# Performance work log

Hardware: AMD Instinct MI355X
Metric: run time of the kernel (lower is better)

## Reference

```python
import jax, jax.numpy as jnp
import numpy as np

B, T, I, H, L = 8192, 256, 28, 10, 2


def setup_inputs() -> dict:
    key = jax.random.key(0)
    ks = jax.random.split(key, 10)
    s_ih0 = 1.0 / np.sqrt(H)
    return {
        "x": jax.random.normal(ks[0], (B, T, I), dtype=jnp.float32),
        "h0": jnp.zeros((L, B, H), dtype=jnp.float32),
        "W_ih_l0": jax.random.uniform(ks[1], (H, I), minval=-s_ih0, maxval=s_ih0),
        "W_hh_l0": jax.random.uniform(ks[2], (H, H), minval=-s_ih0, maxval=s_ih0),
        "b_ih_l0": jax.random.uniform(ks[3], (H,), minval=-s_ih0, maxval=s_ih0),
        "b_hh_l0": jax.random.uniform(ks[4], (H,), minval=-s_ih0, maxval=s_ih0),
        "W_ih_l1": jax.random.uniform(ks[5], (H, H), minval=-s_ih0, maxval=s_ih0),
        "W_hh_l1": jax.random.uniform(ks[6], (H, H), minval=-s_ih0, maxval=s_ih0),
        "b_ih_l1": jax.random.uniform(ks[7], (H,), minval=-s_ih0, maxval=s_ih0),
        "b_hh_l1": jax.random.uniform(ks[8], (H,), minval=-s_ih0, maxval=s_ih0),
    }


def reference(x, h0, W_ih_l0, W_hh_l0, b_ih_l0, b_hh_l0,
              W_ih_l1, W_hh_l1, b_ih_l1, b_hh_l1):
    # torch RNN (tanh): h_t = tanh(x_t @ W_ih^T + b_ih + h_{t-1} @ W_hh^T + b_hh)
    # Precompute layer-0 input projections for all timesteps (big GEMM up front).
    xw0 = jnp.einsum('bti,hi->tbh', x, W_ih_l0) + (b_ih_l0 + b_hh_l0)  # [T,B,H]
    b1 = b_ih_l1 + b_hh_l1

    def step(carry, xw0_t):
        h_0, h_1 = carry
        h_0 = jnp.tanh(xw0_t + h_0 @ W_hh_l0.T)
        h_1 = jnp.tanh(h_0 @ W_ih_l1.T + b1 + h_1 @ W_hh_l1.T)
        return (h_0, h_1), h_1

    (hT_0, hT_1), out_tbh = jax.lax.scan(step, (h0[0], h0[1]), xw0)
    output = jnp.transpose(out_tbh, (1, 0, 2))          # [B,T,H] (batch_first)
    h_final = jnp.stack([hT_0, hT_1], axis=0)           # [2,B,H]
    return output, h_final
```

## Files before the change

### kernel.cpp

```cpp
#include <hip/hip_runtime.h>

#define B_ 8192
#define T_ 256
#define I_ 28
#define H_ 10

#define OUT_MAIN (B_ * T_ * H_)
#define BH (B_ * H_)

typedef __bf16 bf16x8 __attribute__((ext_vector_type(8)));
typedef float f32x16 __attribute__((ext_vector_type(16)));
typedef float f32x4  __attribute__((ext_vector_type(4)));
union W4u { unsigned int w[4]; bf16x8 v; };

__device__ __forceinline__ float fast_tanh(float x) {
    float e = __builtin_amdgcn_exp2f(x * 2.885390081777927f);
    return __builtin_fmaf(-2.0f, __builtin_amdgcn_rcpf(e + 1.0f), 1.0f);
}

__device__ __forceinline__ unsigned short f2bf(float f) {
    unsigned u = __float_as_uint(f);
    unsigned r = ((u >> 16) & 1) + 0x7fff;
    return (unsigned short)((u + r) >> 16);
}

__device__ __forceinline__ void cvtpair(float f0, float f1, unsigned& dh, unsigned& dl) {
    asm("v_cvt_pk_bf16_f32 %0, %1, %2" : "=v"(dh) : "v"(f0), "v"(f1));
    float r0 = f0 - __uint_as_float(dh << 16);
    float r1 = f1 - __uint_as_float(dh & 0xffff0000u);
    asm("v_cvt_pk_bf16_f32 %0, %1, %2" : "=v"(dl) : "v"(r0), "v"(r1));
}

#define REBUILD(vv0,vv1,vv2,vv3,vv4,vv5, DST) { \
    unsigned t01, t23, t45, w3 = 0; \
    asm("v_cvt_pk_bf16_f32 %0, %1, %2" : "=v"(t01) : "v"(vv0), "v"(vv1)); \
    asm("v_cvt_pk_bf16_f32 %0, %1, %2" : "=v"(t23) : "v"(vv2), "v"(vv3)); \
    asm("v_cvt_pk_bf16_f32 %0, %1, %2" : "=v"(t45) : "v"(vv4), "v"(vv5)); \
    asm volatile("s_nop 1" : "+v"(t01), "+v"(t23), "+v"(t45)); \
    asm("v_permlane32_swap_b32 %0, %1" : "+v"(t01), "+v"(t45)); \
    asm("v_permlane32_swap_b32 %0, %1" : "+v"(t23), "+v"(w3)); \
    W4u nb_; nb_.w[0]=t01; nb_.w[1]=t23; nb_.w[2]=t45; nb_.w[3]=w3; \
    DST = nb_.v; }

#define GLD4o(dst, addr, OFF) \
    asm volatile("global_load_dwordx4 %0, %1, off offset:" #OFF : "=v"(dst) : "v"(addr));

#define LOADX(SA, SB, SC, SD, tt) { \
    const float* a0_ = xrow + (long)(tt) * I_ + 8 * h; \
    const float* a1_ = xrow + (long)(tt) * I_ + 20; \
    GLD4o(SA, a0_, 0) \
    GLD4o(SB, a0_, 16) \
    GLD4o(SC, a0_, 64) \
    GLD4o(SD, a1_, 0) }

#define WAITX(SA, SB, SC, SD, N) \
    asm volatile("s_waitcnt vmcnt(" #N ")" : "+v"(SA), "+v"(SB), "+v"(SC), "+v"(SD));

#define MAKEXC(SA, SB, SC, SD) { \
    W4u xhA, xlA, xhB, xlB; \
    cvtpair(SA[0], SA[1], xhA.w[0], xlA.w[0]); \
    cvtpair(SA[2], SA[3], xhA.w[1], xlA.w[1]); \
    cvtpair(SB[0], SB[1], xhA.w[2], xlA.w[2]); \
    cvtpair(SB[2], SB[3], xhA.w[3], xlA.w[3]); \
    cvtpair(SC[0], SC[1], xhB.w[0], xlB.w[0]); \
    cvtpair(SC[2], SC[3], xhB.w[1], xlB.w[1]); \
    cvtpair(SD[0], SD[1], xhB.w[2], xlB.w[2]); \
    cvtpair(SD[2], SD[3], xhB.w[3], xlB.w[3]); \
    f32x16 xcA = __builtin_amdgcn_mfma_f32_32x32x16_bf16(Axh0, xlA.v, C0SEED, 0,0,0); \
    f32x16 xcB = __builtin_amdgcn_mfma_f32_32x32x16_bf16(Axl0, xhA.v, ZERO16, 0,0,0); \
    f32x16 xcC = __builtin_amdgcn_mfma_f32_32x32x16_bf16(Axh0, xhA.v, ZERO16, 0,0,0); \
    xcA = __builtin_amdgcn_mfma_f32_32x32x16_bf16(Axh1, xlB.v, xcA, 0,0,0); \
    xcB = __builtin_amdgcn_mfma_f32_32x32x16_bf16(Axl1, xhB.v, xcB, 0,0,0); \
    xcC = __builtin_amdgcn_mfma_f32_32x32x16_bf16(Axh1, xhB.v, xcC, 0,0,0); \
    XC[0]=xcA[0]+xcB[0]+xcC[0]; XC[1]=xcA[1]+xcB[1]+xcC[1]; \
    XC[2]=xcA[2]+xcB[2]+xcC[2]; XC[3]=xcA[3]+xcB[3]+xcC[3]; \
    XC[4]=xcA[4]+xcB[4]+xcC[4]; XC[5]=xcA[5]+xcB[5]+xcC[5]; }

#define STEP(s8, PA,PB,PC,PD, NA,NB,NC,ND) { \
    int t = tb + (s8); \
    f32x16 c1a = __builtin_amdgcn_mfma_f32_32x32x16_bf16(Ahh1, Bh1, C1SEED, 0,0,0); \
    f32x16 c0  = __builtin_amdgcn_mfma_f32_32x32x16_bf16(Ahh0, Bh0, XC, 0,0,0); \
    WAITX(NA,NB,NC,ND, 8) \
    v0 = fast_tanh(c0[0]); v1 = fast_tanh(c0[1]); v2 = fast_tanh(c0[2]); \
    v3 = fast_tanh(c0[3]); v4 = fast_tanh(c0[4]); v5 = fast_tanh(c0[5]); \
    REBUILD(v0,v1,v2,v3,v4,v5, Bh0) \
    f32x16 c1 = __builtin_amdgcn_mfma_f32_32x32x16_bf16(Aih1, Bh0, c1a, 0,0,0); \
    MAKEXC(NA,NB,NC,ND) \
    g0 = fast_tanh(c1[0]); g1 = fast_tanh(c1[1]); g2 = fast_tanh(c1[2]); \
    g3 = fast_tanh(c1[3]); g4 = fast_tanh(c1[4]); g5 = fast_tanh(c1[5]); \
    float* op = orow + t * H_; \
    *(float4*)(op + xo) = make_float4(g0, g1, g2, g3); \
    if (!h) *(float2*)(op + 8) = make_float2(g4, g5); \
    REBUILD(g0,g1,g2,g3,g4,g5, Bh1) \
    int tl = (t + 4 < T_) ? (t + 4) : (T_ - 1); \
    LOADX(PA,PB,PC,PD, tl) }

__global__ __launch_bounds__(64)
__attribute__((amdgpu_waves_per_eu(1, 1)))
void rnn_fused(const float* __restrict__ x, const float* __restrict__ h0in,
               const float* __restrict__ Wih0, const float* __restrict__ Whh0,
               const float* __restrict__ bih0, const float* __restrict__ bhh0,
               const float* __restrict__ Wih1, const float* __restrict__ Whh1,
               const float* __restrict__ bih1, const float* __restrict__ bhh1,
               float* __restrict__ out, float* __restrict__ hfin) {
    const int l = threadIdx.x;
    const int n = l & 31, h = l >> 5;
    const int bb = blockIdx.x * 32;
    const int am = n;

    W4u a0u, aiu, ahu;
#pragma unroll
    for (int jj = 0; jj < 4; jj++) {
        int k0 = 8*h + 2*jj, k1 = k0 + 1;
        bool r0 = (am < H_) && (k0 < H_), r1 = (am < H_) && (k1 < H_);
        unsigned lo, hi;
        lo = r0 ? f2bf(Whh0[am*H_+k0]) : 0u; hi = r1 ? f2bf(Whh0[am*H_+k1]) : 0u;
        a0u.w[jj] = lo | (hi<<16);
        lo = r0 ? f2bf(Wih1[am*H_+k0]) : 0u; hi = r1 ? f2bf(Wih1[am*H_+k1]) : 0u;
        aiu.w[jj] = lo | (hi<<16);
        lo = r0 ? f2bf(Whh1[am*H_+k0]) : 0u; hi = r1 ? f2bf(Whh1[am*H_+k1]) : 0u;
        ahu.w[jj] = lo | (hi<<16);
    }
    bf16x8 Ahh0 = a0u.v, Aih1 = aiu.v, Ahh1 = ahu.v;
    asm volatile("" : "+v"(Ahh0), "+v"(Aih1), "+v"(Ahh1));

    W4u xh0u, xh1u, xl0u, xl1u;
#pragma unroll
    for (int s = 0; s < 2; s++) {
#pragma unroll
        for (int jj = 0; jj < 4; jj++) {
            int k0 = 16*s + 8*h + 2*jj, k1 = k0 + 1;
            unsigned short h0b=0, h1b=0, l0b=0, l1b=0;
            if (am < H_ && k0 < I_) {
                float f = Wih0[am*I_+k0];
                h0b = f2bf(f);
                l0b = f2bf(f - __uint_as_float(((unsigned)h0b)<<16));
            }
            if (am < H_ && k1 < I_) {
                float f = Wih0[am*I_+k1];
                h1b = f2bf(f);
                l1b = f2bf(f - __uint_as_float(((unsigned)h1b)<<16));
            }
            unsigned wh = (unsigned)h0b | ((unsigned)h1b<<16);
            unsigned wl = (unsigned)l0b | ((unsigned)l1b<<16);
            if (s==0) { xh0u.w[jj]=wh; xl0u.w[jj]=wl; }
            else      { xh1u.w[jj]=wh; xl1u.w[jj]=wl; }
        }
    }
    bf16x8 Axh0 = xh0u.v, Axh1 = xh1u.v, Axl0 = xl0u.v, Axl1 = xl1u.v;
    asm volatile("" : "+v"(Axh0), "+v"(Axh1), "+v"(Axl0), "+v"(Axl1));

    f32x16 C0SEED, C1SEED, ZERO16;
#pragma unroll
    for (int r = 0; r < 16; r++) { C0SEED[r] = 0.f; C1SEED[r] = 0.f; ZERO16[r] = 0.f; }
#pragma unroll
    for (int r = 0; r < 6; r++) {
        int mm = (r & 3) + 8 * (r >> 2) + 4 * h;
        if (mm < H_) {
            C0SEED[r] = bih0[mm] + bhh0[mm];
            C1SEED[r] = bih1[mm] + bhh1[mm];
        }
    }
    asm volatile("" : "+v"(C0SEED), "+v"(C1SEED), "+v"(ZERO16));

    W4u b0u, b1u;
#pragma unroll
    for (int jj = 0; jj < 4; jj++) {
        int k0 = 8*h + 2*jj, k1 = k0 + 1;
        float f0 = (k0 < H_) ? h0in[(bb + n) * H_ + k0] : 0.f;
        float f1 = (k1 < H_) ? h0in[(bb + n) * H_ + k1] : 0.f;
        b0u.w[jj] = (unsigned)f2bf(f0) | ((unsigned)f2bf(f1) << 16);
        f0 = (k0 < H_) ? h0in[BH + (bb + n) * H_ + k0] : 0.f;
        f1 = (k1 < H_) ? h0in[BH + (bb + n) * H_ + k1] : 0.f;
        b1u.w[jj] = (unsigned)f2bf(f0) | ((unsigned)f2bf(f1) << 16);
    }
    bf16x8 Bh0 = b0u.v, Bh1 = b1u.v;

    const float* xrow = x   + (long)(bb + n) * (T_ * I_);
    float*       orow = out + (long)(bb + n) * (T_ * H_);
    const int xo = h ? 4 : 0;

    f32x4 S00, S01, S02, S03, S10, S11, S12, S13;
    f32x4 S20, S21, S22, S23, S30, S31, S32, S33;
    LOADX(S00,S01,S02,S03, 0)
    LOADX(S10,S11,S12,S13, 1)
    LOADX(S20,S21,S22,S23, 2)
    LOADX(S30,S31,S32,S33, 3)

    f32x16 XC = ZERO16;
    WAITX(S00,S01,S02,S03, 12)
    MAKEXC(S00,S01,S02,S03)

    float v0,v1,v2,v3,v4,v5, g0,g1,g2,g3,g4,g5;

    for (int it = 0; it < T_ / 8; it++) {
        int tb = it * 8;
        STEP(0, S00,S01,S02,S03, S10,S11,S12,S13)
        STEP(1, S10,S11,S12,S13, S20,S21,S22,S23)
        STEP(2, S20,S21,S22,S23, S30,S31,S32,S33)
        STEP(3, S30,S31,S32,S33, S00,S01,S02,S03)
        STEP(4, S00,S01,S02,S03, S10,S11,S12,S13)
        STEP(5, S10,S11,S12,S13, S20,S21,S22,S23)
        STEP(6, S20,S21,S22,S23, S30,S31,S32,S33)
        STEP(7, S30,S31,S32,S33, S00,S01,S02,S03)
    }
    float* f0p = hfin + (long)(bb + n) * H_;
    *(float4*)(f0p + xo) = make_float4(v0, v1, v2, v3);
    if (!h) *(float2*)(f0p + 8) = make_float2(v4, v5);
    float* f1p = f0p + BH;
    *(float4*)(f1p + xo) = make_float4(g0, g1, g2, g3);
    if (!h) *(float2*)(f1p + 8) = make_float2(g4, g5);
}

extern "C" void kernel_launch(void* const* d_in, const int* in_sizes, int n_in,
                              void* d_out, int out_size, void* d_ws, size_t ws_size,
                              hipStream_t stream) {
    const float* x     = (const float*)d_in[0];
    const float* h0in  = (const float*)d_in[1];
    const float* Wih0  = (const float*)d_in[2];
    const float* Whh0  = (const float*)d_in[3];
    const float* bih0  = (const float*)d_in[4];
    const float* bhh0  = (const float*)d_in[5];
    const float* Wih1  = (const float*)d_in[6];
    const float* Whh1  = (const float*)d_in[7];
    const float* bih1  = (const float*)d_in[8];
    const float* bhh1  = (const float*)d_in[9];
    float* out = (float*)d_out;

    rnn_fused<<<dim3(B_ / 32), dim3(64), 0, stream>>>(
        x, h0in, Wih0, Whh0, bih0, bhh0, Wih1, Whh1, bih1, bhh1,
        out, out + OUT_MAIN);
}
```

Before: 168.0 us.

## Stage x tiles through double-buffered LDS with coalesced block-wide loads

Replaces the per-lane strided global loads of x rows with cooperative, coalesced dwordx4 loads of contiguous 8-timestep chunks across the 32 batch rows. The chunks go into a double-buffered shared-memory stage, padded to 57 entries per row, and each step reads its slice back from LDS. The intent is to fix poorly coalesced global reads, where each lane fetched scattered 112-byte rows. Output stores also become inline-asm global stores. This costs LDS traffic, extra index arithmetic, and a reliance on the intra-wave ordering of LDS writes and reads with no barrier, which is only valid because the block is a single wave.

Result: no change. 171.0 us (+1.8%).

```diff
diff --git a/kernel.cpp b/kernel.cpp
--- a/kernel.cpp
+++ b/kernel.cpp
@@ -11,6 +11,7 @@
 typedef __bf16 bf16x8 __attribute__((ext_vector_type(8)));
 typedef float f32x16 __attribute__((ext_vector_type(16)));
 typedef float f32x4  __attribute__((ext_vector_type(4)));
+typedef float f32x2  __attribute__((ext_vector_type(2)));
 union W4u { unsigned int w[4]; bf16x8 v; };
 
 __device__ __forceinline__ float fast_tanh(float x) {
@@ -42,21 +43,37 @@
     W4u nb_; nb_.w[0]=t01; nb_.w[1]=t23; nb_.w[2]=t45; nb_.w[3]=w3; \
     DST = nb_.v; }
 
-#define GLD4o(dst, addr, OFF) \
-    asm volatile("global_load_dwordx4 %0, %1, off offset:" #OFF : "=v"(dst) : "v"(addr));
-
-#define LOADX(SA, SB, SC, SD, tt) { \
-    const float* a0_ = xrow + (long)(tt) * I_ + 8 * h; \
-    const float* a1_ = xrow + (long)(tt) * I_ + 20; \
-    GLD4o(SA, a0_, 0) \
-    GLD4o(SB, a0_, 16) \
-    GLD4o(SC, a0_, 64) \
-    GLD4o(SD, a1_, 0) }
-
-#define WAITX(SA, SB, SC, SD, N) \
-    asm volatile("s_waitcnt vmcnt(" #N ")" : "+v"(SA), "+v"(SB), "+v"(SC), "+v"(SD));
-
-#define MAKEXC(SA, SB, SC, SD) { \
+#define GLD4(dst, addr) \
+    asm volatile("global_load_dwordx4 %0, %1, off" : "=v"(dst) : "v"(addr));
+#define WAITL(L, N) asm volatile("s_waitcnt vmcnt(" #N ")" : "+v"(L));
+#define GST4(addr, val) \
+    asm volatile("global_store_dwordx4 %0, %1, off" :: "v"(addr), "v"(val));
+#define GST2(addr, val) \
+    asm volatile("global_store_dwordx2 %0, %1, off" :: "v"(addr), "v"(val));
+
+#define PLOFF(r) ({ int q_ = 64*(r) + l; int b_ = ((q_>>3)*9363)>>16; \
+                    int rm_ = q_ - 56*b_; b_*7168 + rm_*4; })
+#define PDOFF(r) ({ int q_ = 64*(r) + l; int b_ = ((q_>>3)*9363)>>16; \
+                    int rm_ = q_ - 56*b_; b_*57 + rm_; })
+
+#define FILLR(r, L) { \
+    WAITL(L, 8) \
+    stage[fb][PDOFF(r)] = L; \
+    const float* s_ = ((r) < 21) ? (XFa + PLOFF((r)+7)) : (XFb + PLOFF((r)-21)); \
+    GLD4(L, s_) }
+
+#define PFILLR(r, L) { \
+    WAITL(L, 6) \
+    stage[0][PDOFF(r)] = L; \
+    const float* s_ = ((r) < 21) ? (XP0 + PLOFF((r)+7)) : (XP1 + PLOFF((r)-21)); \
+    GLD4(L, s_) }
+
+#define SREAD(bi, trel) { \
+    int ix_ = n*57 + (trel)*7 + 2*h; \
+    SA = stage[bi][ix_];   SB = stage[bi][ix_+1]; \
+    SC = stage[bi][ix_+4]; SD = stage[bi][ix_+5]; }
+
+#define MAKEXC() { \
     W4u xhA, xlA, xhB, xlB; \
     cvtpair(SA[0], SA[1], xhA.w[0], xlA.w[0]); \
     cvtpair(SA[2], SA[3], xhA.w[1], xlA.w[1]); \
@@ -76,24 +93,34 @@
     XC[2]=xcA[2]+xcB[2]+xcC[2]; XC[3]=xcA[3]+xcB[3]+xcC[3]; \
     XC[4]=xcA[4]+xcB[4]+xcC[4]; XC[5]=xcA[5]+xcB[5]+xcC[5]; }
 
-#define STEP(s8, PA,PB,PC,PD, NA,NB,NC,ND) { \
-    int t = tb + (s8); \
+#define STEPCOMMON(t) \
     f32x16 c1a = __builtin_amdgcn_mfma_f32_32x32x16_bf16(Ahh1, Bh1, C1SEED, 0,0,0); \
     f32x16 c0  = __builtin_amdgcn_mfma_f32_32x32x16_bf16(Ahh0, Bh0, XC, 0,0,0); \
-    WAITX(NA,NB,NC,ND, 8) \
     v0 = fast_tanh(c0[0]); v1 = fast_tanh(c0[1]); v2 = fast_tanh(c0[2]); \
     v3 = fast_tanh(c0[3]); v4 = fast_tanh(c0[4]); v5 = fast_tanh(c0[5]); \
     REBUILD(v0,v1,v2,v3,v4,v5, Bh0) \
-    f32x16 c1 = __builtin_amdgcn_mfma_f32_32x32x16_bf16(Aih1, Bh0, c1a, 0,0,0); \
-    MAKEXC(NA,NB,NC,ND) \
+    f32x16 c1 = __builtin_amdgcn_mfma_f32_32x32x16_bf16(Aih1, Bh0, c1a, 0,0,0);
+
+#define STEPTAIL(t) \
     g0 = fast_tanh(c1[0]); g1 = fast_tanh(c1[1]); g2 = fast_tanh(c1[2]); \
     g3 = fast_tanh(c1[3]); g4 = fast_tanh(c1[4]); g5 = fast_tanh(c1[5]); \
-    float* op = orow + t * H_; \
-    *(float4*)(op + xo) = make_float4(g0, g1, g2, g3); \
-    if (!h) *(float2*)(op + 8) = make_float2(g4, g5); \
-    REBUILD(g0,g1,g2,g3,g4,g5, Bh1) \
-    int tl = (t + 4 < T_) ? (t + 4) : (T_ - 1); \
-    LOADX(PA,PB,PC,PD, tl) }
+    { f32x4 gv = {g0,g1,g2,g3}; GST4(orow + (t)*H_ + xo, gv) } \
+    if (!h) { f32x2 gw = {g4,g5}; GST2(orow + (t)*H_ + 8, gw) } \
+    REBUILD(g0,g1,g2,g3,g4,g5, Bh1)
+
+#define STEP(s8, RA,RB,RC,RD) { \
+    STEPCOMMON(tb+(s8)) \
+    SREAD(cb, (s8)+1) \
+    MAKEXC() \
+    STEPTAIL(tb+(s8)) \
+    FILLR(4*(s8)+0, RA) FILLR(4*(s8)+1, RB) \
+    FILLR(4*(s8)+2, RC) FILLR(4*(s8)+3, RD) }
+
+#define STEP7 { \
+    STEPCOMMON(tb+7) \
+    SREAD(fb, 0) \
+    MAKEXC() \
+    STEPTAIL(tb+7) }
 
 __global__ __launch_bounds__(64)
 __attribute__((amdgpu_waves_per_eu(1, 1)))
@@ -107,6 +134,12 @@
     const int n = l & 31, h = l >> 5;
     const int bb = blockIdx.x * 32;
     const int am = n;
+
+    __shared__ f32x4 stage[2][1824];
+    if (l < 32) {
+        f32x4 z = {0.f, 0.f, 0.f, 0.f};
+        stage[0][l*57 + 56] = z; stage[1][l*57 + 56] = z;
+    }
 
     W4u a0u, aiu, ahu;
 #pragma unroll
@@ -176,33 +209,42 @@
     }
     bf16x8 Bh0 = b0u.v, Bh1 = b1u.v;
 
-    const float* xrow = x   + (long)(bb + n) * (T_ * I_);
+    const float* xf   = x   + (long)bb * (T_ * I_);
     float*       orow = out + (long)(bb + n) * (T_ * H_);
     const int xo = h ? 4 : 0;
 
-    f32x4 S00, S01, S02, S03, S10, S11, S12, S13;
-    f32x4 S20, S21, S22, S23, S30, S31, S32, S33;
-    LOADX(S00,S01,S02,S03, 0)
-    LOADX(S10,S11,S12,S13, 1)
-    LOADX(S20,S21,S22,S23, 2)
-    LOADX(S30,S31,S32,S33, 3)
-
-    f32x16 XC = ZERO16;
-    WAITX(S00,S01,S02,S03, 12)
-    MAKEXC(S00,S01,S02,S03)
+    f32x4 L0, L1, L2, L3, L4, L5, L6, SA, SB, SC, SD;
+    const float* XP0 = xf;
+    const float* XP1 = xf + 224;
+    GLD4(L0, XP0 + PLOFF(0)) GLD4(L1, XP0 + PLOFF(1)) GLD4(L2, XP0 + PLOFF(2))
+    GLD4(L3, XP0 + PLOFF(3)) GLD4(L4, XP0 + PLOFF(4)) GLD4(L5, XP0 + PLOFF(5))
+    GLD4(L6, XP0 + PLOFF(6))
+    PFILLR(0,L0)  PFILLR(1,L1)  PFILLR(2,L2)  PFILLR(3,L3)
+    PFILLR(4,L4)  PFILLR(5,L5)  PFILLR(6,L6)  PFILLR(7,L0)
+    PFILLR(8,L1)  PFILLR(9,L2)  PFILLR(10,L3) PFILLR(11,L4)
+    PFILLR(12,L5) PFILLR(13,L6) PFILLR(14,L0) PFILLR(15,L1)
+    PFILLR(16,L2) PFILLR(17,L3) PFILLR(18,L4) PFILLR(19,L5)
+    PFILLR(20,L6) PFILLR(21,L0) PFILLR(22,L1) PFILLR(23,L2)
+    PFILLR(24,L3) PFILLR(25,L4) PFILLR(26,L5) PFILLR(27,L6)
+
+    f32x16 XC;
+    { SREAD(0, 0) MAKEXC() }
 
     float v0,v1,v2,v3,v4,v5, g0,g1,g2,g3,g4,g5;
 
-    for (int it = 0; it < T_ / 8; it++) {
-        int tb = it * 8;
-        STEP(0, S00,S01,S02,S03, S10,S11,S12,S13)
-        STEP(1, S10,S11,S12,S13, S20,S21,S22,S23)
-        STEP(2, S20,S21,S22,S23, S30,S31,S32,S33)
-        STEP(3, S30,S31,S32,S33, S00,S01,S02,S03)
-        STEP(4, S00,S01,S02,S03, S10,S11,S12,S13)
-        STEP(5, S10,S11,S12,S13, S20,S21,S22,S23)
-        STEP(6, S20,S21,S22,S23, S30,S31,S32,S33)
-        STEP(7, S30,S31,S32,S33, S00,S01,S02,S03)
+    for (int k = 0; k < 32; k++) {
+        int tb = k * 8;
+        int cb = k & 1, fb = cb ^ 1;
+        const float* XFa = xf + (long)((k+1 < 32 ? k+1 : 31)) * 224;
+        const float* XFb = xf + (long)((k+2 < 32 ? k+2 : 31)) * 224;
+        STEP(0, L0,L1,L2,L3)
+        STEP(1, L4,L5,L6,L0)
+        STEP(2, L1,L2,L3,L4)
+        STEP(3, L5,L6,L0,L1)
+        STEP(4, L2,L3,L4,L5)
+        STEP(5, L6,L0,L1,L2)
+        STEP(6, L3,L4,L5,L6)
+        STEP7
     }
     float* f0p = hfin + (long)(bb + n) * H_;
     *(float4*)(f0p + xo) = make_float4(v0, v1, v2, v3);
```
